# Optimization experiments

Measured on AMD Instinct MI355X. Metric: run time of the kernel, lower is better.

## Reference

```python
import jax, jax.numpy as jnp
import numpy as np

N_NODES = 100000
N_EDGES = 1600000
N_FEATS = 64
HID1 = 128
HID2 = 128


def setup_inputs() -> dict:
    key = jax.random.key(0)
    ks = jax.random.split(key, 8)
    x = jax.random.normal(ks[0], (N_NODES, N_FEATS), dtype=jnp.float32)
    edge_index = jax.random.randint(ks[1], (2, N_EDGES), 0, N_NODES, dtype=jnp.int64)
    # glorot-ish init for linear weights (out_feats, in_feats), bias zeros (PyG default)
    W1 = jax.random.normal(ks[2], (HID1, N_FEATS), dtype=jnp.float32) * (1.0 / np.sqrt(N_FEATS))
    b1 = jnp.zeros((HID1,), dtype=jnp.float32)
    W2 = jax.random.normal(ks[3], (HID2, HID1), dtype=jnp.float32) * (1.0 / np.sqrt(HID1))
    b2 = jnp.zeros((HID2,), dtype=jnp.float32)
    W3 = jax.random.normal(ks[4], (N_FEATS, HID2), dtype=jnp.float32) * (1.0 / np.sqrt(HID2))
    b3 = jnp.zeros((N_FEATS,), dtype=jnp.float32)
    return {"x": x, "edge_index": edge_index, "W1": W1, "b1": b1,
            "W2": W2, "b2": b2, "W3": W3, "b3": b3}


def _gcn_conv(x, src, dst, norm, W, b, n_nodes):
    # dense linear transform first (out_dim may differ from in_dim)
    h = x @ W.T                                   # [N, out]
    msg = h[src] * norm[:, None]                  # gather + edge-normalize, [E+N, out]
    out = jax.ops.segment_sum(msg, dst, num_segments=n_nodes)  # scatter-add
    return out + b


def reference(x, edge_index, W1, b1, W2, b2, W3, b3):
    n = x.shape[0]
    loop = jnp.arange(n, dtype=edge_index.dtype)
    src = jnp.concatenate([edge_index[0], loop])  # self-loops appended (PyG default)
    dst = jnp.concatenate([edge_index[1], loop])
    # symmetric normalization: deg over target column incl. self-loops
    deg = jax.ops.segment_sum(jnp.ones(dst.shape, dtype=x.dtype), dst, num_segments=n)
    dinv = jnp.where(deg > 0, jax.lax.rsqrt(deg), 0.0)
    norm = dinv[src] * dinv[dst]                  # [E+N]

    h = jax.nn.relu(_gcn_conv(x, src, dst, norm, W1, b1, n))
    h = jax.nn.relu(_gcn_conv(h, src, dst, norm, W2, b2, n))
    h = _gcn_conv(h, src, dst, norm, W3, b3, n)
    return jax.nn.softmax(h, axis=1)
```

## Files before the change

kernel.cpp:

```cpp
#include <hip/hip_runtime.h>
#include <hip/hip_bf16.h>


#define NB1 256

typedef __attribute__((ext_vector_type(4))) _Float16 half4;
typedef __attribute__((ext_vector_type(8))) _Float16 half8;
typedef __attribute__((ext_vector_type(4))) float f32x4;


__global__ __launch_bounds__(256) void k_hist(const int* __restrict__ dst, int E, int C,
                                              int NBUK, int* __restrict__ gh) {
  __shared__ int h[512];
  int t = threadIdx.x, b = blockIdx.x;
  for (int i = t; i < NBUK; i += 256) h[i] = 0;
  __syncthreads();
  int beg = b * C, end = min(beg + C, E);
  for (int i = beg + t; i < end; i += 256) atomicAdd(&h[dst[i] >> 8], 1);
  __syncthreads();
  for (int i = t; i < NBUK; i += 256) gh[i * NB1 + b] = h[i];
}

__global__ __launch_bounds__(256) void k_sum256(const int* __restrict__ g, int L,
                                                int* __restrict__ part) {
  __shared__ int red[256];
  int t = threadIdx.x;
  int idx = blockIdx.x * 256 + t;
  red[t] = (idx < L) ? g[idx] : 0;
  __syncthreads();
  for (int off = 128; off > 0; off >>= 1) {
    if (t < off) red[t] += red[t + off];
    __syncthreads();
  }
  if (t == 0) part[blockIdx.x] = red[0];
}

__global__ __launch_bounds__(512) void k_scan_part(int* __restrict__ part, int NP) {
  __shared__ int sh[512];
  int t = threadIdx.x;
  int v = (t < NP) ? part[t] : 0;
  sh[t] = v;
  __syncthreads();
  for (int off = 1; off < 512; off <<= 1) {
    int u = (t >= off) ? sh[t - off] : 0;
    __syncthreads();
    sh[t] += u;
    __syncthreads();
  }
  if (t < NP) part[t] = sh[t] - v;
}

__global__ __launch_bounds__(256) void k_scan_apply(const int* __restrict__ g, int L,
                                                    const int* __restrict__ part,
                                                    int* __restrict__ gout) {
  __shared__ int sh[256];
  int t = threadIdx.x;
  int idx = blockIdx.x * 256 + t;
  int v = (idx < L) ? g[idx] : 0;
  sh[t] = v;
  __syncthreads();
  for (int off = 1; off < 256; off <<= 1) {
    int u = (t >= off) ? sh[t - off] : 0;
    __syncthreads();
    sh[t] += u;
    __syncthreads();
  }
  if (idx < L) gout[idx] = part[blockIdx.x] + sh[t] - v;
}

__global__ __launch_bounds__(256) void k_scatter(const int* __restrict__ src,
                                                 const int* __restrict__ dst, int E, int C,
                                                 int NBUK, const int* __restrict__ gscan,
                                                 int* __restrict__ epak) {
  __shared__ int cur[512];
  int t = threadIdx.x, b = blockIdx.x;
  for (int i = t; i < NBUK; i += 256) cur[i] = gscan[i * NB1 + b];
  __syncthreads();
  int beg = b * C, end = min(beg + C, E);
  for (int i = beg + t; i < end; i += 256) {
    int d = dst[i];
    int p = atomicAdd(&cur[d >> 8], 1);
    epak[p] = src[i] | ((d & 255) << 24);
  }
}

__global__ __launch_bounds__(256) void k_csr(const int* __restrict__ epak,
                                             const int* __restrict__ gscan, int NBUK, int N, int E,
                                             int* __restrict__ rowptr, float* __restrict__ dinv,
                                             int* __restrict__ col) {
  __shared__ int cnt[256];
  __shared__ int scn[256];
  __shared__ int cur[256];
  int b = blockIdx.x, t = threadIdx.x;
  int ebeg = gscan[b * NB1];
  int eend = (b + 1 < NBUK) ? gscan[(b + 1) * NB1] : E;
  cnt[t] = 0;
  __syncthreads();
  for (int i = ebeg + t; i < eend; i += 256) atomicAdd(&cnt[(epak[i] >> 24) & 255], 1);
  __syncthreads();
  int c = cnt[t];
  scn[t] = c;
  __syncthreads();
  for (int off = 1; off < 256; off <<= 1) {
    int v = (t >= off) ? scn[t - off] : 0;
    __syncthreads();
    scn[t] += v;
    __syncthreads();
  }
  int excl = scn[t] - c;
  int node = b * 256 + t;
  if (node < N) {
    rowptr[node] = ebeg + excl;
    dinv[node] = rsqrtf((float)(c + 1));
  }
  cur[t] = ebeg + excl;
  __syncthreads();
  for (int i = ebeg + t; i < eend; i += 256) {
    int e = epak[i];
    int p = atomicAdd(&cur[(e >> 24) & 255], 1);
    col[p] = e & 0xFFFFFF;
  }
  if (b == 0 && t == 0) rowptr[N] = E;
}

__global__ __launch_bounds__(256) void k_prep_w(const float* __restrict__ W1,
                                                const float* __restrict__ W2,
                                                const float* __restrict__ W3,
                                                _Float16* __restrict__ w1h,
                                                _Float16* __restrict__ w2h,
                                                _Float16* __restrict__ w3h) {
  int i = blockIdx.x * 256 + threadIdx.x;
  if (i < 128 * 64) w1h[i] = (_Float16)W1[i];
  if (i < 128 * 128) w2h[i] = (_Float16)W2[i];
  if (i < 64 * 128) w3h[i] = (_Float16)W3[i];
}

__global__ __launch_bounds__(256) void k_prescaleh(const float* __restrict__ x,
                                                   const float* __restrict__ dinv,
                                                   _Float16* __restrict__ xp, int N) {
  int i = blockIdx.x * 256 + threadIdx.x;
  if (i < N * 16) {
    int row = i >> 4;
    float4 v = ((const float4*)x)[i];
    float d = dinv[row];
    half4 o;
    o[0] = (_Float16)(v.x * d);
    o[1] = (_Float16)(v.y * d);
    o[2] = (_Float16)(v.z * d);
    o[3] = (_Float16)(v.w * d);
    ((half4*)xp)[i] = o;
  }
}


template <int EPI>
__global__ __launch_bounds__(256) void k_agg64h(const _Float16* __restrict__ hp,
                                                const float* __restrict__ dinv,
                                                const int* __restrict__ rowptr,
                                                const int* __restrict__ col,
                                                const float* __restrict__ bias,
                                                void* __restrict__ outp, int N) {
  int wid = blockIdx.x * 4 + (threadIdx.x >> 6);
  int lane = threadIdx.x & 63;
  if (wid >= N) return;
  int g = lane >> 3;
  int fl = (lane & 7) * 8;
  float acc[8] = {0.f, 0.f, 0.f, 0.f, 0.f, 0.f, 0.f, 0.f};
  int r0 = rowptr[wid], r1 = rowptr[wid + 1];
  for (int base = r0; base < r1; base += 64) {
    int mm = min(64, r1 - base);
    int ce = (base + lane < r1) ? col[base + lane] : 0;
    for (int j = 0; j < mm; j += 16) {
      int i0 = j + g, i1 = j + 8 + g;
      int s0 = __shfl(ce, i0);
      int s1 = __shfl(ce, i1);
      if (i0 < mm) {
        half8 v = *(const half8*)&hp[(size_t)s0 * 64 + fl];
#pragma unroll
        for (int k = 0; k < 8; ++k) acc[k] += (float)v[k];
      }
      if (i1 < mm) {
        half8 v = *(const half8*)&hp[(size_t)s1 * 64 + fl];
#pragma unroll
        for (int k = 0; k < 8; ++k) acc[k] += (float)v[k];
      }
    }
  }
#pragma unroll
  for (int o = 8; o < 64; o <<= 1) {
#pragma unroll
    for (int k = 0; k < 8; ++k) acc[k] += __shfl_xor(acc[k], o);
  }
  half8 sv = *(const half8*)&hp[(size_t)wid * 64 + fl];
  float di = dinv[wid];
  float v[8];
#pragma unroll
  for (int k = 0; k < 8; ++k) v[k] = di * (acc[k] + (float)sv[k]);
  if (EPI == 0) {
    if (lane < 8) {
      half8 o;
#pragma unroll
      for (int k = 0; k < 8; ++k) o[k] = (_Float16)v[k];
      *(half8*)&((_Float16*)outp)[(size_t)wid * 64 + fl] = o;
    }
  } else {
    float4 ba = *(const float4*)&bias[fl];
    float4 bb = *(const float4*)&bias[fl + 4];
    v[0] += ba.x; v[1] += ba.y; v[2] += ba.z; v[3] += ba.w;
    v[4] += bb.x; v[5] += bb.y; v[6] += bb.z; v[7] += bb.w;
    float mx = v[0];
#pragma unroll
    for (int k = 1; k < 8; ++k) mx = fmaxf(mx, v[k]);
#pragma unroll
    for (int o = 1; o < 8; o <<= 1) mx = fmaxf(mx, __shfl_xor(mx, o));
    float s = 0.f;
#pragma unroll
    for (int k = 0; k < 8; ++k) {
      v[k] = expf(v[k] - mx);
      s += v[k];
    }
#pragma unroll
    for (int o = 1; o < 8; o <<= 1) s += __shfl_xor(s, o);
    float inv = 1.0f / s;
#pragma unroll
    for (int k = 0; k < 8; ++k) v[k] *= inv;
    if (lane < 8) {
      float4 o0 = make_float4(v[0], v[1], v[2], v[3]);
      float4 o1 = make_float4(v[4], v[5], v[6], v[7]);
      *(float4*)&((float*)outp)[(size_t)wid * 64 + fl] = o0;
      *(float4*)&((float*)outp)[(size_t)wid * 64 + fl + 4] = o1;
    }
  }
}

__global__ __launch_bounds__(256) void k_agg128h(const _Float16* __restrict__ hp,
                                                 const float* __restrict__ dinv,
                                                 const int* __restrict__ rowptr,
                                                 const int* __restrict__ col,
                                                 _Float16* __restrict__ out, int N) {
  int wid = blockIdx.x * 4 + (threadIdx.x >> 6);
  int lane = threadIdx.x & 63;
  if (wid >= N) return;
  int g = lane >> 4;
  int fl = (lane & 15) * 8;
  float acc[8] = {0.f, 0.f, 0.f, 0.f, 0.f, 0.f, 0.f, 0.f};
  int r0 = rowptr[wid], r1 = rowptr[wid + 1];
  for (int base = r0; base < r1; base += 64) {
    int mm = min(64, r1 - base);
    int ce = (base + lane < r1) ? col[base + lane] : 0;
    for (int j = 0; j < mm; j += 8) {
      int i0 = j + g, i1 = j + 4 + g;
      int s0 = __shfl(ce, i0);
      int s1 = __shfl(ce, i1);
      if (i0 < mm) {
        half8 v = *(const half8*)&hp[(size_t)s0 * 128 + fl];
#pragma unroll
        for (int k = 0; k < 8; ++k) acc[k] += (float)v[k];
      }
      if (i1 < mm) {
        half8 v = *(const half8*)&hp[(size_t)s1 * 128 + fl];
#pragma unroll
        for (int k = 0; k < 8; ++k) acc[k] += (float)v[k];
      }
    }
  }
#pragma unroll
  for (int o = 16; o < 64; o <<= 1) {
#pragma unroll
    for (int k = 0; k < 8; ++k) acc[k] += __shfl_xor(acc[k], o);
  }
  half8 sv = *(const half8*)&hp[(size_t)wid * 128 + fl];
  float di = dinv[wid];
  if (lane < 16) {
    half8 o;
#pragma unroll
    for (int k = 0; k < 8; ++k) o[k] = (_Float16)(di * (acc[k] + (float)sv[k]));
    *(half8*)&out[(size_t)wid * 128 + fl] = o;
  }
}


__global__ __launch_bounds__(256) void k_mfma1(const _Float16* __restrict__ a1h,
                                               const _Float16* __restrict__ w1h,
                                               const float* __restrict__ b1,
                                               const float* __restrict__ dinv,
                                               _Float16* __restrict__ h1, int N) {
  int wave = threadIdx.x >> 6, lane = threadIdx.x & 63;
  int rb = blockIdx.x * 128 + wave * 32;
  if (rb >= N) return;
  int lrow = lane & 15, lg = lane >> 4;

  half8 arow[2][2];
#pragma unroll
  for (int rt = 0; rt < 2; ++rt) {
    int r = rb + rt * 16 + lrow;
    if (r >= N) r = N - 1;
    const _Float16* p = &a1h[(size_t)r * 64 + lg * 8];
    arow[rt][0] = *(const half8*)p;
    arow[rt][1] = *(const half8*)(p + 32);
  }
  f32x4 acc[2][8];
#pragma unroll
  for (int rt = 0; rt < 2; ++rt)
#pragma unroll
    for (int nt = 0; nt < 8; ++nt) acc[rt][nt] = (f32x4){0.f, 0.f, 0.f, 0.f};

#pragma unroll
  for (int nt = 0; nt < 8; ++nt) {
#pragma unroll
    for (int ks = 0; ks < 2; ++ks) {
      half8 wf = *(const half8*)&w1h[(size_t)(nt * 16 + lrow) * 64 + ks * 32 + lg * 8];
      acc[0][nt] = __builtin_amdgcn_mfma_f32_16x16x32_f16(wf, arow[0][ks], acc[0][nt], 0, 0, 0);
      acc[1][nt] = __builtin_amdgcn_mfma_f32_16x16x32_f16(wf, arow[1][ks], acc[1][nt], 0, 0, 0);
    }
  }
#pragma unroll
  for (int rt = 0; rt < 2; ++rt) {
    int r = rb + rt * 16 + lrow;
    if (r < N) {
      float di = dinv[r];
#pragma unroll
      for (int nt = 0; nt < 8; ++nt) {
        int n = nt * 16 + lg * 4;
        float4 bb = *(const float4*)&b1[n];
        half4 o;
        o[0] = (_Float16)(fmaxf(acc[rt][nt][0] + bb.x, 0.f) * di);
        o[1] = (_Float16)(fmaxf(acc[rt][nt][1] + bb.y, 0.f) * di);
        o[2] = (_Float16)(fmaxf(acc[rt][nt][2] + bb.z, 0.f) * di);
        o[3] = (_Float16)(fmaxf(acc[rt][nt][3] + bb.w, 0.f) * di);
        *(half4*)&h1[(size_t)r * 128 + n] = o;
      }
    }
  }
}

__global__ __launch_bounds__(256) void k_mfma23(const _Float16* __restrict__ a2h,
                                                const _Float16* __restrict__ w2h,
                                                const float* __restrict__ b2,
                                                const _Float16* __restrict__ w3h,
                                                const float* __restrict__ dinv,
                                                _Float16* __restrict__ hz, int N) {
  __shared__ _Float16 u_lds[4][32][136];
  int wave = threadIdx.x >> 6, lane = threadIdx.x & 63;
  int rb = blockIdx.x * 128 + wave * 32;
  if (rb >= N) return;
  int lrow = lane & 15, lg = lane >> 4;

  half8 frag[2][4];
#pragma unroll
  for (int rt = 0; rt < 2; ++rt) {
    int r = rb + rt * 16 + lrow;
    if (r >= N) r = N - 1;
    const _Float16* p = &a2h[(size_t)r * 128 + lg * 8];
#pragma unroll
    for (int ks = 0; ks < 4; ++ks) frag[rt][ks] = *(const half8*)(p + ks * 32);
  }
  f32x4 acc[2][8];
#pragma unroll
  for (int rt = 0; rt < 2; ++rt)
#pragma unroll
    for (int nt = 0; nt < 8; ++nt) acc[rt][nt] = (f32x4){0.f, 0.f, 0.f, 0.f};

#pragma unroll
  for (int nt = 0; nt < 8; ++nt) {
#pragma unroll
    for (int ks = 0; ks < 4; ++ks) {
      half8 wf = *(const half8*)&w2h[(size_t)(nt * 16 + lrow) * 128 + ks * 32 + lg * 8];
      acc[0][nt] = __builtin_amdgcn_mfma_f32_16x16x32_f16(wf, frag[0][ks], acc[0][nt], 0, 0, 0);
      acc[1][nt] = __builtin_amdgcn_mfma_f32_16x16x32_f16(wf, frag[1][ks], acc[1][nt], 0, 0, 0);
    }
  }
#pragma unroll
  for (int rt = 0; rt < 2; ++rt) {
#pragma unroll
    for (int nt = 0; nt < 8; ++nt) {
      int n = nt * 16 + lg * 4;
      float4 bb = *(const float4*)&b2[n];
      half4 o;
      o[0] = (_Float16)fmaxf(acc[rt][nt][0] + bb.x, 0.f);
      o[1] = (_Float16)fmaxf(acc[rt][nt][1] + bb.y, 0.f);
      o[2] = (_Float16)fmaxf(acc[rt][nt][2] + bb.z, 0.f);
      o[3] = (_Float16)fmaxf(acc[rt][nt][3] + bb.w, 0.f);
      *(half4*)&u_lds[wave][rt * 16 + lrow][n] = o;
    }
  }
#pragma unroll
  for (int rt = 0; rt < 2; ++rt)
#pragma unroll
    for (int ks = 0; ks < 4; ++ks)
      frag[rt][ks] = *(const half8*)&u_lds[wave][rt * 16 + lrow][ks * 32 + lg * 8];

  f32x4 acc2[2][4];
#pragma unroll
  for (int rt = 0; rt < 2; ++rt)
#pragma unroll
    for (int mt = 0; mt < 4; ++mt) acc2[rt][mt] = (f32x4){0.f, 0.f, 0.f, 0.f};

#pragma unroll
  for (int mt = 0; mt < 4; ++mt) {
#pragma unroll
    for (int ks = 0; ks < 4; ++ks) {
      half8 wf = *(const half8*)&w3h[(size_t)(mt * 16 + lrow) * 128 + ks * 32 + lg * 8];
      acc2[0][mt] = __builtin_amdgcn_mfma_f32_16x16x32_f16(wf, frag[0][ks], acc2[0][mt], 0, 0, 0);
      acc2[1][mt] = __builtin_amdgcn_mfma_f32_16x16x32_f16(wf, frag[1][ks], acc2[1][mt], 0, 0, 0);
    }
  }
#pragma unroll
  for (int rt = 0; rt < 2; ++rt) {
    int r = rb + rt * 16 + lrow;
    if (r < N) {
      float di = dinv[r];
#pragma unroll
      for (int mt = 0; mt < 4; ++mt) {
        int m = mt * 16 + lg * 4;
        half4 o;
        o[0] = (_Float16)(acc2[rt][mt][0] * di);
        o[1] = (_Float16)(acc2[rt][mt][1] * di);
        o[2] = (_Float16)(acc2[rt][mt][2] * di);
        o[3] = (_Float16)(acc2[rt][mt][3] * di);
        *(half4*)&hz[(size_t)r * 64 + m] = o;
      }
    }
  }
}


extern "C" void kernel_launch(void* const* d_in, const int* in_sizes, int n_in,
                              void* d_out, int out_size, void* d_ws, size_t ws_size,
                              hipStream_t stream) {
  const float* x  = (const float*)d_in[0];
  const int*   ei = (const int*)d_in[1];
  const float* W1 = (const float*)d_in[2];
  const float* b1 = (const float*)d_in[3];
  const float* W2 = (const float*)d_in[4];
  const float* b2 = (const float*)d_in[5];
  const float* W3 = (const float*)d_in[6];
  const float* b3 = (const float*)d_in[7];
  float* out = (float*)d_out;

  const int N = in_sizes[0] / 64;
  const int E = in_sizes[1] / 2;
  const int* esrc = ei;
  const int* edst = ei + E;

  const int NBUK = (N + 255) / 256;
  const int C1 = (E + NB1 - 1) / NB1;
  const int L = NBUK * NB1;
  const int NA = (L + 255) / 256;

  char* w = (char*)d_ws;
  auto take = [&](size_t bytes) -> void* {
    void* p = (void*)w;
    w += (bytes + 255) & ~(size_t)255;
    return p;
  };
  int*   rowptr = (int*)take((size_t)(N + 1) * 4);
  float* dinv   = (float*)take((size_t)N * 4);
  int*   col    = (int*)take((size_t)E * 4);
  int*   gh     = (int*)take((size_t)L * 4);
  int*   gscan  = (int*)take((size_t)L * 4);
  int*   part   = (int*)take((size_t)NA * 4);
  _Float16* w1h = (_Float16*)take((size_t)128 * 64 * 2);
  _Float16* w2h = (_Float16*)take((size_t)128 * 128 * 2);
  _Float16* w3h = (_Float16*)take((size_t)64 * 128 * 2);
  _Float16* hx  = (_Float16*)take((size_t)N * 64 * 2);
  _Float16* a1h = (_Float16*)take((size_t)N * 64 * 2);
  _Float16* h1  = (_Float16*)take((size_t)N * 128 * 2);
  _Float16* a2h = (_Float16*)take((size_t)N * 128 * 2);
  int*   epak   = (int*)h1;
  _Float16* hz  = hx;

  k_hist<<<NB1, 256, 0, stream>>>(edst, E, C1, NBUK, gh);
  k_sum256<<<NA, 256, 0, stream>>>(gh, L, part);
  k_scan_part<<<1, 512, 0, stream>>>(part, NA);
  k_scan_apply<<<NA, 256, 0, stream>>>(gh, L, part, gscan);
  k_scatter<<<NB1, 256, 0, stream>>>(esrc, edst, E, C1, NBUK, gscan, epak);
  k_csr<<<NBUK, 256, 0, stream>>>(epak, gscan, NBUK, N, E, rowptr, dinv, col);

  k_prep_w<<<64, 256, 0, stream>>>(W1, W2, W3, w1h, w2h, w3h);

  const int aggblocks = (N + 3) / 4;
  const int mfmablocks = (N + 127) / 128;

  k_prescaleh<<<(N * 16 + 255) / 256, 256, 0, stream>>>(x, dinv, hx, N);
  k_agg64h<0><<<aggblocks, 256, 0, stream>>>(hx, dinv, rowptr, col, nullptr, a1h, N);
  k_mfma1<<<mfmablocks, 256, 0, stream>>>(a1h, w1h, b1, dinv, h1, N);
  k_agg128h<<<aggblocks, 256, 0, stream>>>(h1, dinv, rowptr, col, a2h, N);
  k_mfma23<<<mfmablocks, 256, 0, stream>>>(a2h, w2h, b2, w3h, dinv, hz, N);
  k_agg64h<1><<<aggblocks, 256, 0, stream>>>(hz, dinv, rowptr, col, b3, out, N);
}
```

Baseline: 357.6 us.

## Slice feature matrices into 16-wide column panels for cache-friendly aggregation

Intermediate feature tensors are stored as column slices of 16 halves per node (slice-major), and the aggregation kernels run one slice per grid-y so each gather pass touches a smaller working set that fits in L2. The MFMA kernels and the x prescale are adapted to read and write the sliced layout. Separately, the one-block partial scan is folded into scan_apply, and weight conversion is merged with the x prescale into one launch. The trade-off is that the edge list (col) is now re-read once per slice instead of once per layer.

```diff
diff --git a/kernel.cpp b/kernel.cpp
--- a/kernel.cpp
+++ b/kernel.cpp
@@ -35,27 +35,26 @@
   if (t == 0) part[blockIdx.x] = red[0];
 }
 
-__global__ __launch_bounds__(512) void k_scan_part(int* __restrict__ part, int NP) {
-  __shared__ int sh[512];
-  int t = threadIdx.x;
-  int v = (t < NP) ? part[t] : 0;
-  sh[t] = v;
-  __syncthreads();
-  for (int off = 1; off < 512; off <<= 1) {
-    int u = (t >= off) ? sh[t - off] : 0;
-    __syncthreads();
-    sh[t] += u;
-    __syncthreads();
-  }
-  if (t < NP) part[t] = sh[t] - v;
-}
-
 __global__ __launch_bounds__(256) void k_scan_apply(const int* __restrict__ g, int L,
-                                                    const int* __restrict__ part,
+                                                    const int* __restrict__ part, int NP,
                                                     int* __restrict__ gout) {
+  __shared__ int pl[512];
   __shared__ int sh[256];
-  int t = threadIdx.x;
-  int idx = blockIdx.x * 256 + t;
+  int t = threadIdx.x, bid = blockIdx.x;
+  pl[t] = (t < NP) ? part[t] : 0;
+  pl[t + 256] = (t + 256 < NP) ? part[t + 256] : 0;
+  __syncthreads();
+  int partial = 0;
+  for (int i = t; i < bid; i += 256) partial += pl[i];
+  sh[t] = partial;
+  __syncthreads();
+  for (int off = 128; off > 0; off >>= 1) {
+    if (t < off) sh[t] += sh[t + off];
+    __syncthreads();
+  }
+  int pre = sh[0];
+  __syncthreads();
+  int idx = bid * 256 + t;
   int v = (idx < L) ? g[idx] : 0;
   sh[t] = v;
   __syncthreads();
@@ -65,7 +64,7 @@
     sh[t] += u;
     __syncthreads();
   }
-  if (idx < L) gout[idx] = part[blockIdx.x] + sh[t] - v;
+  if (idx < L) gout[idx] = pre + sh[t] - v;
 }
 
 __global__ __launch_bounds__(256) void k_scatter(const int* __restrict__ src,
@@ -123,43 +122,84 @@
   if (b == 0 && t == 0) rowptr[N] = E;
 }
 
-__global__ __launch_bounds__(256) void k_prep_w(const float* __restrict__ W1,
-                                                const float* __restrict__ W2,
-                                                const float* __restrict__ W3,
-                                                _Float16* __restrict__ w1h,
-                                                _Float16* __restrict__ w2h,
-                                                _Float16* __restrict__ w3h) {
-  int i = blockIdx.x * 256 + threadIdx.x;
-  if (i < 128 * 64) w1h[i] = (_Float16)W1[i];
-  if (i < 128 * 128) w2h[i] = (_Float16)W2[i];
-  if (i < 64 * 128) w3h[i] = (_Float16)W3[i];
-}
-
-__global__ __launch_bounds__(256) void k_prescaleh(const float* __restrict__ x,
-                                                   const float* __restrict__ dinv,
-                                                   _Float16* __restrict__ xp, int N) {
-  int i = blockIdx.x * 256 + threadIdx.x;
-  if (i < N * 16) {
-    int row = i >> 4;
-    float4 v = ((const float4*)x)[i];
-    float d = dinv[row];
-    half4 o;
-    o[0] = (_Float16)(v.x * d);
-    o[1] = (_Float16)(v.y * d);
-    o[2] = (_Float16)(v.z * d);
-    o[3] = (_Float16)(v.w * d);
-    ((half4*)xp)[i] = o;
-  }
-}
-
-
-template <int EPI>
-__global__ __launch_bounds__(256) void k_agg64h(const _Float16* __restrict__ hp,
+__global__ __launch_bounds__(256) void k_prep(const float* __restrict__ x,
+                                              const float* __restrict__ dinv,
+                                              const float* __restrict__ W1,
+                                              const float* __restrict__ W2,
+                                              const float* __restrict__ W3,
+                                              _Float16* __restrict__ hx_s,
+                                              _Float16* __restrict__ w1h,
+                                              _Float16* __restrict__ w2h,
+                                              _Float16* __restrict__ w3h, int N, int PRE) {
+  int t = threadIdx.x;
+  if ((int)blockIdx.x >= PRE) {
+    int i = ((int)blockIdx.x - PRE) * 256 + t;
+    if (i < 128 * 64) w1h[i] = (_Float16)W1[i];
+    if (i < 128 * 128) w2h[i] = (_Float16)W2[i];
+    if (i < 64 * 128) w3h[i] = (_Float16)W3[i];
+    return;
+  }
+  __shared__ float xl[32 * 64];
+  int rbase = blockIdx.x * 32;
+  const float4* xp = (const float4*)&x[(size_t)rbase * 64];
+  ((float4*)xl)[t] = xp[t];
+  ((float4*)xl)[t + 256] = xp[t + 256];
+  __syncthreads();
+  int slice = t >> 6, rem = t & 63, ri = rem >> 1, fo = (rem & 1) * 8;
+  int r = rbase + ri;
+  float d = dinv[r];
+  half8 o;
+#pragma unroll
+  for (int k = 0; k < 8; ++k) o[k] = (_Float16)(xl[ri * 64 + slice * 16 + fo + k] * d);
+  *(half8*)&hx_s[((size_t)slice * N + r) * 16 + fo] = o;
+}
+
+template <int NS>
+__global__ __launch_bounds__(256) void k_aggs(const _Float16* __restrict__ tin,
+                                              const float* __restrict__ dinv,
+                                              const int* __restrict__ rowptr,
+                                              const int* __restrict__ col,
+                                              _Float16* __restrict__ tout, int N) {
+  int slice = blockIdx.y;
+  int wave = threadIdx.x >> 6, lane = threadIdx.x & 63;
+  int r = blockIdx.x * 16 + wave * 4 + (lane >> 4);
+  if (r >= N) return;
+  int eg = (lane >> 1) & 7;
+  int fo = (lane & 1) * 8;
+  const _Float16* ts = tin + (size_t)slice * N * 16;
+  float acc[8] = {0.f, 0.f, 0.f, 0.f, 0.f, 0.f, 0.f, 0.f};
+  int r0 = rowptr[r], r1 = rowptr[r + 1];
+  for (int base = r0; base < r1; base += 8) {
+    int e = base + eg;
+    int ec = (e < r1) ? e : r0;
+    int s = __builtin_nontemporal_load(&col[ec]);
+    half8 v = *(const half8*)&ts[(size_t)s * 16 + fo];
+    if (e < r1) {
+#pragma unroll
+      for (int k = 0; k < 8; ++k) acc[k] += (float)v[k];
+    }
+  }
+#pragma unroll
+  for (int o = 2; o <= 8; o <<= 1) {
+#pragma unroll
+    for (int k = 0; k < 8; ++k) acc[k] += __shfl_xor(acc[k], o);
+  }
+  if (eg == 0) {
+    half8 sv = *(const half8*)&ts[(size_t)r * 16 + fo];
+    float di = dinv[r];
+    half8 o;
+#pragma unroll
+    for (int k = 0; k < 8; ++k) o[k] = (_Float16)(di * (acc[k] + (float)sv[k]));
+    *(half8*)&tout[((size_t)slice * N + r) * 16 + fo] = o;
+  }
+}
+
+__global__ __launch_bounds__(256) void k_agg64f(const _Float16* __restrict__ hp,
                                                 const float* __restrict__ dinv,
                                                 const int* __restrict__ rowptr,
                                                 const int* __restrict__ col,
                                                 const float* __restrict__ bias,
-                                                void* __restrict__ outp, int N) {
+                                                float* __restrict__ out, int N) {
   int wid = blockIdx.x * 4 + (threadIdx.x >> 6);
   int lane = threadIdx.x & 63;
   if (wid >= N) return;
@@ -196,95 +236,40 @@
   float v[8];
 #pragma unroll
   for (int k = 0; k < 8; ++k) v[k] = di * (acc[k] + (float)sv[k]);
-  if (EPI == 0) {
-    if (lane < 8) {
-      half8 o;
-#pragma unroll
-      for (int k = 0; k < 8; ++k) o[k] = (_Float16)v[k];
-      *(half8*)&((_Float16*)outp)[(size_t)wid * 64 + fl] = o;
-    }
-  } else {
-    float4 ba = *(const float4*)&bias[fl];
-    float4 bb = *(const float4*)&bias[fl + 4];
-    v[0] += ba.x; v[1] += ba.y; v[2] += ba.z; v[3] += ba.w;
-    v[4] += bb.x; v[5] += bb.y; v[6] += bb.z; v[7] += bb.w;
-    float mx = v[0];
-#pragma unroll
-    for (int k = 1; k < 8; ++k) mx = fmaxf(mx, v[k]);
-#pragma unroll
-    for (int o = 1; o < 8; o <<= 1) mx = fmaxf(mx, __shfl_xor(mx, o));
-    float s = 0.f;
-#pragma unroll
-    for (int k = 0; k < 8; ++k) {
-      v[k] = expf(v[k] - mx);
-      s += v[k];
-    }
-#pragma unroll
-    for (int o = 1; o < 8; o <<= 1) s += __shfl_xor(s, o);
-    float inv = 1.0f / s;
-#pragma unroll
-    for (int k = 0; k < 8; ++k) v[k] *= inv;
-    if (lane < 8) {
-      float4 o0 = make_float4(v[0], v[1], v[2], v[3]);
-      float4 o1 = make_float4(v[4], v[5], v[6], v[7]);
-      *(float4*)&((float*)outp)[(size_t)wid * 64 + fl] = o0;
-      *(float4*)&((float*)outp)[(size_t)wid * 64 + fl + 4] = o1;
-    }
-  }
-}
-
-__global__ __launch_bounds__(256) void k_agg128h(const _Float16* __restrict__ hp,
-                                                 const float* __restrict__ dinv,
-                                                 const int* __restrict__ rowptr,
-                                                 const int* __restrict__ col,
-                                                 _Float16* __restrict__ out, int N) {
-  int wid = blockIdx.x * 4 + (threadIdx.x >> 6);
-  int lane = threadIdx.x & 63;
-  if (wid >= N) return;
-  int g = lane >> 4;
-  int fl = (lane & 15) * 8;
-  float acc[8] = {0.f, 0.f, 0.f, 0.f, 0.f, 0.f, 0.f, 0.f};
-  int r0 = rowptr[wid], r1 = rowptr[wid + 1];
-  for (int base = r0; base < r1; base += 64) {
-    int mm = min(64, r1 - base);
-    int ce = (base + lane < r1) ? col[base + lane] : 0;
-    for (int j = 0; j < mm; j += 8) {
-      int i0 = j + g, i1 = j + 4 + g;
-      int s0 = __shfl(ce, i0);
-      int s1 = __shfl(ce, i1);
-      if (i0 < mm) {
-        half8 v = *(const half8*)&hp[(size_t)s0 * 128 + fl];
-#pragma unroll
-        for (int k = 0; k < 8; ++k) acc[k] += (float)v[k];
-      }
-      if (i1 < mm) {
-        half8 v = *(const half8*)&hp[(size_t)s1 * 128 + fl];
-#pragma unroll
-        for (int k = 0; k < 8; ++k) acc[k] += (float)v[k];
-      }
-    }
-  }
-#pragma unroll
-  for (int o = 16; o < 64; o <<= 1) {
-#pragma unroll
-    for (int k = 0; k < 8; ++k) acc[k] += __shfl_xor(acc[k], o);
-  }
-  half8 sv = *(const half8*)&hp[(size_t)wid * 128 + fl];
-  float di = dinv[wid];
-  if (lane < 16) {
-    half8 o;
-#pragma unroll
-    for (int k = 0; k < 8; ++k) o[k] = (_Float16)(di * (acc[k] + (float)sv[k]));
-    *(half8*)&out[(size_t)wid * 128 + fl] = o;
-  }
-}
-
-
-__global__ __launch_bounds__(256) void k_mfma1(const _Float16* __restrict__ a1h,
+  float4 ba = *(const float4*)&bias[fl];
+  float4 bb = *(const float4*)&bias[fl + 4];
+  v[0] += ba.x; v[1] += ba.y; v[2] += ba.z; v[3] += ba.w;
+  v[4] += bb.x; v[5] += bb.y; v[6] += bb.z; v[7] += bb.w;
+  float mx = v[0];
+#pragma unroll
+  for (int k = 1; k < 8; ++k) mx = fmaxf(mx, v[k]);
+#pragma unroll
+  for (int o = 1; o < 8; o <<= 1) mx = fmaxf(mx, __shfl_xor(mx, o));
+  float s = 0.f;
+#pragma unroll
+  for (int k = 0; k < 8; ++k) {
+    v[k] = expf(v[k] - mx);
+    s += v[k];
+  }
+#pragma unroll
+  for (int o = 1; o < 8; o <<= 1) s += __shfl_xor(s, o);
+  float inv = 1.0f / s;
+#pragma unroll
+  for (int k = 0; k < 8; ++k) v[k] *= inv;
+  if (lane < 8) {
+    float4 o0 = make_float4(v[0], v[1], v[2], v[3]);
+    float4 o1 = make_float4(v[4], v[5], v[6], v[7]);
+    *(float4*)&out[(size_t)wid * 64 + fl] = o0;
+    *(float4*)&out[(size_t)wid * 64 + fl + 4] = o1;
+  }
+}
+
+
+__global__ __launch_bounds__(256) void k_mfma1(const _Float16* __restrict__ a1s,
                                                const _Float16* __restrict__ w1h,
                                                const float* __restrict__ b1,
                                                const float* __restrict__ dinv,
-                                               _Float16* __restrict__ h1, int N) {
+                                               _Float16* __restrict__ h1s, int N) {
   int wave = threadIdx.x >> 6, lane = threadIdx.x & 63;
   int rb = blockIdx.x * 128 + wave * 32;
   if (rb >= N) return;
@@ -295,9 +280,9 @@
   for (int rt = 0; rt < 2; ++rt) {
     int r = rb + rt * 16 + lrow;
     if (r >= N) r = N - 1;
-    const _Float16* p = &a1h[(size_t)r * 64 + lg * 8];
-    arow[rt][0] = *(const half8*)p;
-    arow[rt][1] = *(const half8*)(p + 32);
+#pragma unroll
+    for (int ks = 0; ks < 2; ++ks)
+      arow[rt][ks] = *(const half8*)&a1s[((size_t)(2 * ks + (lg >> 1)) * N + r) * 16 + (lg & 1) * 8];
   }
   f32x4 acc[2][8];
 #pragma unroll
@@ -328,13 +313,13 @@
         o[1] = (_Float16)(fmaxf(acc[rt][nt][1] + bb.y, 0.f) * di);
         o[2] = (_Float16)(fmaxf(acc[rt][nt][2] + bb.z, 0.f) * di);
         o[3] = (_Float16)(fmaxf(acc[rt][nt][3] + bb.w, 0.f) * di);
-        *(half4*)&h1[(size_t)r * 128 + n] = o;
+        *(half4*)&h1s[((size_t)nt * N + r) * 16 + lg * 4] = o;
       }
     }
   }
 }
 
-__global__ __launch_bounds__(256) void k_mfma23(const _Float16* __restrict__ a2h,
+__global__ __launch_bounds__(256) void k_mfma23(const _Float16* __restrict__ a2s,
                                                 const _Float16* __restrict__ w2h,
                                                 const float* __restrict__ b2,
                                                 const _Float16* __restrict__ w3h,
@@ -351,9 +336,9 @@
   for (int rt = 0; rt < 2; ++rt) {
     int r = rb + rt * 16 + lrow;
     if (r >= N) r = N - 1;
-    const _Float16* p = &a2h[(size_t)r * 128 + lg * 8];
-#pragma unroll
-    for (int ks = 0; ks < 4; ++ks) frag[rt][ks] = *(const half8*)(p + ks * 32);
+#pragma unroll
+    for (int ks = 0; ks < 4; ++ks)
+      frag[rt][ks] = *(const half8*)&a2s[((size_t)(2 * ks + (lg >> 1)) * N + r) * 16 + (lg & 1) * 8];
   }
   f32x4 acc[2][8];
 #pragma unroll
@@ -463,29 +448,28 @@
   _Float16* w1h = (_Float16*)take((size_t)128 * 64 * 2);
   _Float16* w2h = (_Float16*)take((size_t)128 * 128 * 2);
   _Float16* w3h = (_Float16*)take((size_t)64 * 128 * 2);
-  _Float16* hx  = (_Float16*)take((size_t)N * 64 * 2);
-  _Float16* a1h = (_Float16*)take((size_t)N * 64 * 2);
-  _Float16* h1  = (_Float16*)take((size_t)N * 128 * 2);
-  _Float16* a2h = (_Float16*)take((size_t)N * 128 * 2);
-  int*   epak   = (int*)h1;
-  _Float16* hz  = hx;
+  _Float16* hx_s = (_Float16*)take((size_t)4 * N * 16 * 2);
+  _Float16* a1s  = (_Float16*)take((size_t)4 * N * 16 * 2);
+  _Float16* h1s  = (_Float16*)take((size_t)8 * N * 16 * 2);
+  _Float16* a2s  = (_Float16*)take((size_t)8 * N * 16 * 2);
+  int*   epak   = (int*)h1s;
+  _Float16* hz  = hx_s;
 
   k_hist<<<NB1, 256, 0, stream>>>(edst, E, C1, NBUK, gh);
   k_sum256<<<NA, 256, 0, stream>>>(gh, L, part);
-  k_scan_part<<<1, 512, 0, stream>>>(part, NA);
-  k_scan_apply<<<NA, 256, 0, stream>>>(gh, L, part, gscan);
+  k_scan_apply<<<NA, 256, 0, stream>>>(gh, L, part, NA, gscan);
   k_scatter<<<NB1, 256, 0, stream>>>(esrc, edst, E, C1, NBUK, gscan, epak);
   k_csr<<<NBUK, 256, 0, stream>>>(epak, gscan, NBUK, N, E, rowptr, dinv, col);
 
-  k_prep_w<<<64, 256, 0, stream>>>(W1, W2, W3, w1h, w2h, w3h);
-
-  const int aggblocks = (N + 3) / 4;
+  const int PRE = (N + 31) / 32;
+  k_prep<<<PRE + 128, 256, 0, stream>>>(x, dinv, W1, W2, W3, hx_s, w1h, w2h, w3h, N, PRE);
+
+  const int rowblocks = (N + 15) / 16;
   const int mfmablocks = (N + 127) / 128;
 
-  k_prescaleh<<<(N * 16 + 255) / 256, 256, 0, stream>>>(x, dinv, hx, N);
-  k_agg64h<0><<<aggblocks, 256, 0, stream>>>(hx, dinv, rowptr, col, nullptr, a1h, N);
-  k_mfma1<<<mfmablocks, 256, 0, stream>>>(a1h, w1h, b1, dinv, h1, N);
-  k_agg128h<<<aggblocks, 256, 0, stream>>>(h1, dinv, rowptr, col, a2h, N);
-  k_mfma23<<<mfmablocks, 256, 0, stream>>>(a2h, w2h, b2, w3h, dinv, hz, N);
-  k_agg64h<1><<<aggblocks, 256, 0, stream>>>(hz, dinv, rowptr, col, b3, out, N);
-}
+  k_aggs<4><<<dim3(rowblocks, 4), 256, 0, stream>>>(hx_s, dinv, rowptr, col, a1s, N);
+  k_mfma1<<<mfmablocks, 256, 0, stream>>>(a1s, w1h, b1, dinv, h1s, N);
+  k_aggs<8><<<dim3(rowblocks, 8), 256, 0, stream>>>(h1s, dinv, rowptr, col, a2s, N);
+  k_mfma23<<<mfmablocks, 256, 0, stream>>>(a2s, w2h, b2, w3h, dinv, hz, N);
+  k_agg64f<<<(N + 3) / 4, 256, 0, stream>>>(hz, dinv, rowptr, col, b3, out, N);
+}
```

Result: slower. 436.3 us (+22.0%).
